# Optimization experiments

Measured on AMD Instinct MI355X. Metric: run time of the kernel, lower is better.

The kernel has to match this reference:

```python
import jax, jax.numpy as jnp
import numpy as np

B, L1, L2, H = 8, 384, 384, 128


def _lin(k, out_f, in_f, scale=0.05):
    kw, kb = jax.random.split(k)
    return (jax.random.normal(kw, (out_f, in_f), jnp.float32) * scale,
            jax.random.normal(kb, (out_f,), jnp.float32) * scale)


def setup_inputs() -> dict:
    key = jax.random.key(0)
    ks = jax.random.split(key, 10)
    Wq_w, Wq_b = _lin(ks[2], H, H)
    Wup_w, Wup_b = _lin(ks[3], H, H)
    Wvp_w, Wvp_b = _lin(ks[4], H, H)
    V_w, V_b = _lin(ks[5], 1, H)
    Wg_w, Wg_b = _lin(ks[6], 2 * H, 2 * H)
    W_ih, b_ih = _lin(ks[7], 4 * H, 2 * H)
    W_hh, b_hh = _lin(ks[8], 4 * H, H)
    return {
        "x": jax.random.normal(ks[0], (B, L1, H), jnp.float32),
        "x_mask": jnp.zeros((B, L1), dtype=bool),
        "y": jax.random.normal(ks[1], (B, L2, H), jnp.float32),
        "y_mask": jnp.zeros((B, L2), dtype=bool),
        "Wq_w": Wq_w, "Wq_b": Wq_b,
        "Wup_w": Wup_w, "Wup_b": Wup_b,
        "Wvp_w": Wvp_w, "Wvp_b": Wvp_b,
        "V_w": V_w, "V_b": V_b,
        "Wg_w": Wg_w, "Wg_b": Wg_b,
        "W_ih": W_ih, "W_hh": W_hh, "b_ih": b_ih, "b_hh": b_hh,
    }


def reference(x, x_mask, y, y_mask, Wq_w, Wq_b, Wup_w, Wup_b, Wvp_w, Wvp_b,
              V_w, V_b, Wg_w, Wg_b, W_ih, W_hh, b_ih, b_hh):
    b, l1, h = x.shape
    # projections (torch Linear: x @ W.T + b)
    x_proj = x @ Wup_w.T + Wup_b                      # [B, L1, H]
    y_proj = y @ Wq_w.T + Wq_b                        # [B, L2, H]
    # source feeds a constant zero hidden state into W_vp -> just its bias
    hidden_proj = jnp.zeros((h,), x.dtype) @ Wvp_w.T + Wvp_b  # [H]
    # additive attention scores: V . tanh(xp + yp + hp)
    sum_batch = jnp.tanh(x_proj[:, :, None, :] + y_proj[:, None, :, :] + hidden_proj)  # [B,L1,L2,H]
    s = jnp.einsum('btjh,h->btj', sum_batch, V_w[0]) + V_b[0]  # [B, L1, L2]
    # sum_mask = (1 - x_mask) outer (1 - y_mask)
    xm = 1.0 - x_mask.astype(s.dtype)
    ym = 1.0 - y_mask.astype(s.dtype)
    s = s * (xm[:, :, None] * ym[:, None, :])
    s = jnp.where(y_mask[:, None, :], -jnp.inf, s)
    alpha = jax.nn.softmax(s, axis=-1)                # [B, L1, L2]
    ct = jnp.einsum('btj,bjh->bth', alpha, y)         # [B, L1, H]
    merge = jnp.concatenate([x, ct], axis=2)          # [B, L1, 2H]
    gt = jax.nn.sigmoid(merge @ Wg_w.T + Wg_b)
    lstm_in = gt * merge                              # [B, L1, 2H]
    # single-layer unidirectional LSTM (torch gate order: i, f, g, o)
    gates_x = lstm_in @ W_ih.T + b_ih                 # [B, L1, 4H]

    def step(carry, gx):
        h_t, c_t = carry
        g = gx + h_t @ W_hh.T + b_hh
        i, f, gg, o = jnp.split(g, 4, axis=-1)
        c_n = jax.nn.sigmoid(f) * c_t + jax.nn.sigmoid(i) * jnp.tanh(gg)
        h_n = jax.nn.sigmoid(o) * jnp.tanh(c_n)
        return (h_n, c_n), h_n

    init = (jnp.zeros((b, h), x.dtype), jnp.zeros((b, h), x.dtype))
    _, hs = jax.lax.scan(step, init, jnp.swapaxes(gates_x, 0, 1))  # [L1, B, H]
    return jnp.swapaxes(hs, 0, 1)                     # [B, L1, H]
```

## Files before the change

### kernel.cpp

```cpp
#include <hip/hip_runtime.h>
#include <hip/hip_bf16.h>
#include <math.h>

typedef __attribute__((ext_vector_type(4))) float  float4v;
typedef __attribute__((ext_vector_type(2))) float  float2v;
typedef __attribute__((ext_vector_type(8))) short  short8;

#define B_ 8
#define L_ 384
#define H_ 128

__device__ __forceinline__ float bflo(unsigned int u){ unsigned int t = u << 16; float f; __builtin_memcpy(&f,&t,4); return f; }
__device__ __forceinline__ unsigned short f2bf(float f){
  unsigned int t; __builtin_memcpy(&t,&f,4);
  return (unsigned short)((t + 0x7fffu + ((t>>16)&1u)) >> 16);
}
__device__ __forceinline__ float fsig(float x){ return __fdividef(1.f, 1.f + __expf(-x)); }

__device__ __forceinline__ void barrier_lds(){
  asm volatile("s_waitcnt lgkmcnt(0)\n\ts_barrier" ::: "memory");
}

template<int K>
__device__ __forceinline__ void mfma_rowgemm_body(
    unsigned short* in_s,
    const float* __restrict__ inA, const float* __restrict__ inB,
    const float* __restrict__ W, const float* __restrict__ bias,
    const float* __restrict__ bias2, float* __restrict__ out,
    int Ntotal, int act, int row0, int ob)
{
  constexpr int KP = K + 2;
  const int tid  = threadIdx.x;
  const int w    = tid >> 6;
  const int l    = tid & 63;
  const int c    = l & 15;
  const int quad = l >> 4;

  #pragma unroll
  for (int it = 0; it < K/32; ++it) {
    int idx = it*256 + tid;
    int r = idx / (K/4);
    int k = (idx % (K/4)) * 4;
    float4v f;
    if (inB != nullptr && k >= 128)
      f = *(const float4v*)(inB + (size_t)(row0+r)*128 + (k-128));
    else if (inB != nullptr)
      f = *(const float4v*)(inA + (size_t)(row0+r)*128 + k);
    else
      f = *(const float4v*)(inA + (size_t)(row0+r)*K + k);
    unsigned int p0 = (unsigned int)f2bf(f.x) | ((unsigned int)f2bf(f.y) << 16);
    unsigned int p1 = (unsigned int)f2bf(f.z) | ((unsigned int)f2bf(f.w) << 16);
    *(unsigned int*)&in_s[r*KP + k]     = p0;
    *(unsigned int*)&in_s[r*KP + k + 2] = p1;
  }

  const int n = ob + w*16 + c;
  short8 bfr[K/32];
  #pragma unroll
  for (int kt = 0; kt < K/32; ++kt) {
    const float* src = W + (size_t)n*K + kt*32 + quad*8;
    float4v f0 = *(const float4v*)(src);
    float4v f1 = *(const float4v*)(src + 4);
    short8 v;
    v[0]=(short)f2bf(f0[0]); v[1]=(short)f2bf(f0[1]); v[2]=(short)f2bf(f0[2]); v[3]=(short)f2bf(f0[3]);
    v[4]=(short)f2bf(f1[0]); v[5]=(short)f2bf(f1[1]); v[6]=(short)f2bf(f1[2]); v[7]=(short)f2bf(f1[3]);
    bfr[kt] = v;
  }
  __syncthreads();

  const float4v z4 = {0.f,0.f,0.f,0.f};
  float4v acc0 = z4, acc1 = z4;
  #pragma unroll
  for (int kt = 0; kt < K/32; ++kt) {
    short8 a0 = *(const short8*)&in_s[(c     )*KP + kt*32 + quad*8];
    short8 a1 = *(const short8*)&in_s[(16 + c)*KP + kt*32 + quad*8];
    acc0 = __builtin_amdgcn_mfma_f32_16x16x32_bf16(a0, bfr[kt], acc0, 0,0,0);
    acc1 = __builtin_amdgcn_mfma_f32_16x16x32_bf16(a1, bfr[kt], acc1, 0,0,0);
  }

  const float C2 = 2.8853900817779268f;
  float bv = bias[n] + (bias2 ? bias2[n] : 0.f);
  #pragma unroll
  for (int mt = 0; mt < 2; ++mt) {
    float4v A = mt ? acc1 : acc0;
    #pragma unroll
    for (int r = 0; r < 4; ++r) {
      int m = mt*16 + quad*4 + r;
      float val = A[r] + bv;
      if (act == 2) {
        float mg = bflo((unsigned int)in_s[m*KP + n]);
        val = fsig(val) * mg;
      }
      if (act == 4)
        val = __builtin_amdgcn_exp2f(C2 * val);
      if (act == 3)
        out[(size_t)(row0+m)*Ntotal + (n & 127)*4 + (n >> 7)] = val;
      else
        out[(size_t)(row0+m)*Ntotal + n] = val;
    }
  }
}

template<int K>
__global__ __launch_bounds__(256) void mfma_rowgemm_kernel(
    const float* __restrict__ inA, const float* __restrict__ inB,
    const float* __restrict__ W, const float* __restrict__ bias,
    const float* __restrict__ bias2, float* __restrict__ out,
    int Ntotal, int act)
{
  __shared__ __align__(16) unsigned short in_s[32*(K+2)];
  mfma_rowgemm_body<K>(in_s, inA, inB, W, bias, bias2, out,
                       Ntotal, act, blockIdx.x*32, blockIdx.y*64);
}

__global__ __launch_bounds__(256) void proj_mfma_kernel(
    const float* __restrict__ x, const float* __restrict__ y,
    const float* __restrict__ Wup_w, const float* __restrict__ Wup_b,
    const float* __restrict__ Wq_w, const float* __restrict__ Wq_b,
    const float* __restrict__ Wvp_b,
    float* __restrict__ xp, float* __restrict__ yp)
{
  __shared__ __align__(16) unsigned short in_s[32*130];
  int bx = blockIdx.x;
  if (bx < 192)
    mfma_rowgemm_body<128>(in_s, x, nullptr, Wup_w, Wup_b, nullptr,
                           xp, 128, 4, (bx>>1)*32, (bx&1)*64);
  else {
    bx -= 192;
    mfma_rowgemm_body<128>(in_s, y, nullptr, Wq_w, Wq_b, Wvp_b,
                           yp, 128, 4, (bx>>1)*32, (bx&1)*64);
  }
}

__global__ __launch_bounds__(256) void attn_kernel(
    const float* __restrict__ xp, const float* __restrict__ yp,
    const float* __restrict__ y, const unsigned char* __restrict__ xmask,
    const unsigned char* __restrict__ ymask, const float* __restrict__ Vw,
    const float* __restrict__ Vb,
    float* __restrict__ ctp0, float* __restrict__ ctp1,
    float* __restrict__ ml)
{
  __shared__ __align__(16) float xp_s[8][128];
  __shared__ __align__(16) float v2_s[128];
  __shared__ __align__(16) float yp_s[32][132];
  __shared__ __align__(16) float yc_s[32][132];
  __shared__ float xm_s[8];
  __shared__ float ym_s[32];
  __shared__ float sv_s;
  const int tid = threadIdx.x;
  const int b   = blockIdx.y;
  const int t0  = blockIdx.x * 8;
  const int jh  = blockIdx.z;
  {
    int r = tid >> 5, k4 = (tid & 31) * 4;
    float4v f = *(const float4v*)(xp + ((size_t)(b*L_ + t0 + r))*H_ + k4);
    *(float4v*)&xp_s[r][k4] = f;
    if (tid < 32) {
      float4v v = *(const float4v*)(Vw + tid*4);
      float4v v2; v2[0]=2.f*v[0]; v2[1]=2.f*v[1]; v2[2]=2.f*v[2]; v2[3]=2.f*v[3];
      *(float4v*)&v2_s[tid*4] = v2;
    }
    if (tid < 8) xm_s[tid] = xmask[b*L_ + t0 + tid] ? 0.f : 1.f;
  }
  __syncthreads();
  if (tid < 32) {
    float4v v = *(const float4v*)&v2_s[tid*4];
    float sm = (v[0]+v[1]) + (v[2]+v[3]);
    #pragma unroll
    for (int off = 16; off >= 1; off >>= 1) sm += __shfl_xor(sm, off);
    if (tid == 0) sv_s = 0.5f*sm + Vb[0];
  }

  float4v rp[4], ry[4];
  unsigned char ymb = 0;
  {
    #pragma unroll
    for (int it = 0; it < 4; ++it) {
      int idx = it*256 + tid; int r = idx >> 5; int k4 = (idx & 31) * 4;
      size_t base = ((size_t)(b*L_ + jh*192 + r))*H_ + k4;
      rp[it] = *(const float4v*)(yp + base);
      ry[it] = *(const float4v*)(y + base);
    }
    if (tid < 32) ymb = ymask[b*L_ + jh*192 + tid];
  }

  const int t = tid >> 5, u = tid & 31;
  float mrun = -__builtin_inff(), lrun = 0.f;
  float a0=0.f, a1=0.f, a2=0.f, a3=0.f;
  float svc = 0.f, xmv = 0.f;

  for (int c = 0; c < 6; ++c) {
    __syncthreads();
    #pragma unroll
    for (int it = 0; it < 4; ++it) {
      int idx = it*256 + tid; int r = idx >> 5; int k4 = (idx & 31) * 4;
      *(float4v*)&yp_s[r][k4] = rp[it];
      *(float4v*)&yc_s[r][k4] = ry[it];
    }
    if (tid < 32) ym_s[tid] = ymb ? 0.f : 1.f;
    __syncthreads();
    if (c == 0) { svc = sv_s; xmv = xm_s[t]; }
    if (c < 5) {
      #pragma unroll
      for (int it = 0; it < 4; ++it) {
        int idx = it*256 + tid; int r = idx >> 5; int k4 = (idx & 31) * 4;
        size_t base = ((size_t)(b*L_ + jh*192 + (c+1)*32 + r))*H_ + k4;
        rp[it] = *(const float4v*)(yp + base);
        ry[it] = *(const float4v*)(y + base);
      }
      if (tid < 32) ymb = ymask[b*L_ + jh*192 + (c+1)*32 + tid];
    }

    float sA = 0.f, sB = 0.f;
    {
      const float* yr = yp_s[u];
      const float* xr = xp_s[t];
      #pragma unroll 4
      for (int k = 0; k < 128; k += 4) {
        float4v yv = *(const float4v*)&yr[k];
        float4v xv = *(const float4v*)&xr[k];
        float4v vv = *(const float4v*)&v2_s[k];
        sA -= vv[0] * __builtin_amdgcn_rcpf(__builtin_fmaf(xv[0], yv[0], 1.f));
        sB -= vv[1] * __builtin_amdgcn_rcpf(__builtin_fmaf(xv[1], yv[1], 1.f));
        sA -= vv[2] * __builtin_amdgcn_rcpf(__builtin_fmaf(xv[2], yv[2], 1.f));
        sB -= vv[3] * __builtin_amdgcn_rcpf(__builtin_fmaf(xv[3], yv[3], 1.f));
      }
    }
    float ymv = ym_s[u];
    float s = (svc + sA + sB) * xmv * ymv;
    if (ymv == 0.f) s = -__builtin_inff();
    float mc = s;
    #pragma unroll
    for (int off = 16; off >= 1; off >>= 1) mc = fmaxf(mc, __shfl_xor(mc, off));
    float mnew = fmaxf(mrun, mc);
    float p  = __expf(s - mnew);
    float sc = __expf(mrun - mnew);
    float ps = p;
    #pragma unroll
    for (int off = 16; off >= 1; off >>= 1) ps += __shfl_xor(ps, off);
    lrun = lrun * sc + ps;
    mrun = mnew;
    a0 *= sc; a1 *= sc; a2 *= sc; a3 *= sc;
    #pragma unroll 8
    for (int j = 0; j < 32; ++j) {
      float pv = __shfl(p, j, 32);
      float4v yv = *(const float4v*)&yc_s[j][u*4];
      a0 += pv*yv[0]; a1 += pv*yv[1]; a2 += pv*yv[2]; a3 += pv*yv[3];
    }
  }
  const int row = b*L_ + t0 + t;
  float* ctp = jh ? ctp1 : ctp0;
  float4v ov; ov[0]=a0; ov[1]=a1; ov[2]=a2; ov[3]=a3;
  *(float4v*)(ctp + (size_t)row*H_ + u*4) = ov;
  if (u == 0) {
    ml[(jh*2+0)*3072 + row] = mrun;
    ml[(jh*2+1)*3072 + row] = lrun;
  }
}

__global__ __launch_bounds__(256) void attn_merge_kernel(
    const float* __restrict__ ctp0, const float* __restrict__ ctp1,
    const float* __restrict__ ml, float* __restrict__ ct)
{
  const int tid = threadIdx.x;
  const int row = blockIdx.x*8 + (tid >> 5);
  const int c4  = (tid & 31) * 4;
  float m0 = ml[row],        l0 = ml[3072 + row];
  float m1 = ml[2*3072+row], l1 = ml[3*3072 + row];
  float m  = fmaxf(m0, m1);
  float e0 = __expf(m0 - m), e1 = __expf(m1 - m);
  float inv = __fdividef(1.f, l0*e0 + l1*e1);
  float4v v0 = *(const float4v*)(ctp0 + (size_t)row*H_ + c4);
  float4v v1 = *(const float4v*)(ctp1 + (size_t)row*H_ + c4);
  float4v r;
  r[0] = (v0[0]*e0 + v1[0]*e1)*inv;
  r[1] = (v0[1]*e0 + v1[1]*e1)*inv;
  r[2] = (v0[2]*e0 + v1[2]*e1)*inv;
  r[3] = (v0[3]*e0 + v1[3]*e1)*inv;
  *(float4v*)(ct + (size_t)row*H_ + c4) = r;
}

__global__ __launch_bounds__(512) void lstm_kernel(
    const float* __restrict__ gx, const float* __restrict__ Whh,
    float* __restrict__ out)
{
  __shared__ __align__(16) unsigned short h_s[2][128];
  const int tid  = threadIdx.x;
  const int b    = blockIdx.x;
  const int w    = tid >> 6;
  const int l    = tid & 63;
  const int col  = l & 15;
  const int quad = l >> 4;

  short8 bf[4][4];
  #pragma unroll
  for (int nt = 0; nt < 4; ++nt) {
    const int n = nt*128 + w*16 + col;
    #pragma unroll
    for (int kt = 0; kt < 4; ++kt) {
      const int k0 = kt*32 + quad*8;
      const float* src = Whh + (size_t)n*H_ + k0;
      float4v f0 = *(const float4v*)(src);
      float4v f1 = *(const float4v*)(src + 4);
      short8 v;
      v[0]=(short)f2bf(f0[0]); v[1]=(short)f2bf(f0[1]); v[2]=(short)f2bf(f0[2]); v[3]=(short)f2bf(f0[3]);
      v[4]=(short)f2bf(f1[0]); v[5]=(short)f2bf(f1[1]); v[6]=(short)f2bf(f1[2]); v[7]=(short)f2bf(f1[3]);
      bf[nt][kt] = v;
    }
  }

  if (tid < 128) { h_s[0][tid] = 0; h_s[1][tid] = 0; }
  float cst = 0.f;
  const int goff = w*16 + col;
  const float* gbase = gx + (size_t)b*L_*512 + goff*4;
  float* outp = out + (size_t)b*L_*H_ + goff;
  float4v gbuf[4];
  #pragma unroll
  for (int s = 0; s < 4; ++s)
    gbuf[s] = *(const float4v*)(gbase + (size_t)s*512);
  const float4v z4 = {0.f,0.f,0.f,0.f};
  const float NL2E = -1.4426950408889634f;
  const float P2L2E = 2.8853900817779268f;
  __syncthreads();

  for (int t4 = 0; t4 < L_; t4 += 4) {
    #pragma unroll
    for (int s = 0; s < 4; ++s) {
      const int tstep = t4 + s;
      const unsigned short* hb = h_s[s & 1];
      short8 a[4];
      #pragma unroll
      for (int kt=0;kt<4;++kt) a[kt] = *(const short8*)&hb[kt*32 + quad*8];
      float4v c0 = z4, c1 = z4, c2 = z4, c3 = z4;
      #pragma unroll
      for (int kt=0;kt<4;++kt) {
        c0 = __builtin_amdgcn_mfma_f32_16x16x32_bf16(a[kt], bf[0][kt], c0, 0,0,0);
        c1 = __builtin_amdgcn_mfma_f32_16x16x32_bf16(a[kt], bf[1][kt], c1, 0,0,0);
        c2 = __builtin_amdgcn_mfma_f32_16x16x32_bf16(a[kt], bf[2][kt], c2, 0,0,0);
        c3 = __builtin_amdgcn_mfma_f32_16x16x32_bf16(a[kt], bf[3][kt], c3, 0,0,0);
      }
      float g0 = c0[0] + gbuf[s][0];
      float g1 = c1[0] + gbuf[s][1];
      float g2 = c2[0] + gbuf[s][2];
      float g3 = c3[0] + gbuf[s][3];
      if (tstep + 4 < L_)
        gbuf[s] = *(const float4v*)(gbase + (size_t)(tstep+4)*512);
      if (quad == 0) {
        float ig = __builtin_amdgcn_rcpf(1.f + __builtin_amdgcn_exp2f(NL2E*g0));
        float fg = __builtin_amdgcn_rcpf(1.f + __builtin_amdgcn_exp2f(NL2E*g1));
        float gg = 1.f - 2.f*__builtin_amdgcn_rcpf(__builtin_amdgcn_exp2f(P2L2E*g2) + 1.f);
        float og = __builtin_amdgcn_rcpf(1.f + __builtin_amdgcn_exp2f(NL2E*g3));
        cst = fg*cst + ig*gg;
        float hn = og * (1.f - 2.f*__builtin_amdgcn_rcpf(__builtin_amdgcn_exp2f(P2L2E*cst) + 1.f));
        outp[(size_t)tstep*H_] = hn;
        h_s[(s+1)&1][goff] = f2bf(hn);
      }
      barrier_lds();
    }
  }
}

extern "C" void kernel_launch(void* const* d_in, const int* in_sizes, int n_in,
                              void* d_out, int out_size, void* d_ws, size_t ws_size,
                              hipStream_t stream)
{
  (void)in_sizes; (void)n_in; (void)out_size; (void)ws_size;
  const float* x     = (const float*)d_in[0];
  const unsigned char* xm = (const unsigned char*)d_in[1];
  const float* y     = (const float*)d_in[2];
  const unsigned char* ym = (const unsigned char*)d_in[3];
  const float* Wq_w  = (const float*)d_in[4];
  const float* Wq_b  = (const float*)d_in[5];
  const float* Wup_w = (const float*)d_in[6];
  const float* Wup_b = (const float*)d_in[7];
  const float* Wvp_b = (const float*)d_in[9];
  const float* V_w   = (const float*)d_in[10];
  const float* V_b   = (const float*)d_in[11];
  const float* Wg_w  = (const float*)d_in[12];
  const float* Wg_b  = (const float*)d_in[13];
  const float* W_ih  = (const float*)d_in[14];
  const float* W_hh  = (const float*)d_in[15];
  const float* b_ih  = (const float*)d_in[16];
  const float* b_hh  = (const float*)d_in[17];
  float* out = (float*)d_out;

  float* wsf    = (float*)d_ws;
  float* xp_ws  = wsf;
  float* yp_ws  = xp_ws + 393216;
  float* ct_ws  = yp_ws + 393216;
  float* li_ws  = ct_ws + 393216;
  float* gx_ws  = li_ws + 786432;
  float* ct2_ws = gx_ws + 1572864;
  float* ml_ws  = ct2_ws + 393216;

  proj_mfma_kernel<<<dim3(384),256,0,stream>>>(x, y, Wup_w, Wup_b, Wq_w, Wq_b, Wvp_b, xp_ws, yp_ws);
  attn_kernel<<<dim3(48,8,2),256,0,stream>>>(xp_ws, yp_ws, y, xm, ym, V_w, V_b, ct_ws, ct2_ws, ml_ws);
  attn_merge_kernel<<<dim3(384),256,0,stream>>>(ct_ws, ct2_ws, ml_ws, ct_ws);
  mfma_rowgemm_kernel<256><<<dim3(96,4),256,0,stream>>>(x, ct_ws, Wg_w, Wg_b, nullptr, li_ws, 256, 2);
  mfma_rowgemm_kernel<256><<<dim3(96,8),256,0,stream>>>(li_ws, nullptr, W_ih, b_ih, b_hh, gx_ws, 512, 3);
  lstm_kernel<<<dim3(8),512,0,stream>>>(gx_ws, W_hh, out);
}
```

Measured before the change: 338.1 us.

## Split attention over four key chunks and fuse partial merge into gate GEMM

The attention kernel now splits the key dimension into four chunks of 96 instead of two of 192, which doubles the grid to raise parallelism. The separate merge kernel is removed, and the gate GEMM now combines the four partial softmax results (max, sum and partial context) while loading its input tile. This removes one launch and one round trip of the context through memory, at the cost of more partial buffers and redundant merge arithmetic in the gate loads. li_ws now reuses the xp buffer to save workspace.

```diff
diff --git a/kernel.cpp b/kernel.cpp
--- a/kernel.cpp
+++ b/kernel.cpp
@@ -24,7 +24,7 @@
 template<int K>
 __device__ __forceinline__ void mfma_rowgemm_body(
     unsigned short* in_s,
-    const float* __restrict__ inA, const float* __restrict__ inB,
+    const float* __restrict__ inA,
     const float* __restrict__ W, const float* __restrict__ bias,
     const float* __restrict__ bias2, float* __restrict__ out,
     int Ntotal, int act, int row0, int ob)
@@ -41,13 +41,7 @@
     int idx = it*256 + tid;
     int r = idx / (K/4);
     int k = (idx % (K/4)) * 4;
-    float4v f;
-    if (inB != nullptr && k >= 128)
-      f = *(const float4v*)(inB + (size_t)(row0+r)*128 + (k-128));
-    else if (inB != nullptr)
-      f = *(const float4v*)(inA + (size_t)(row0+r)*128 + k);
-    else
-      f = *(const float4v*)(inA + (size_t)(row0+r)*K + k);
+    float4v f = *(const float4v*)(inA + (size_t)(row0+r)*K + k);
     unsigned int p0 = (unsigned int)f2bf(f.x) | ((unsigned int)f2bf(f.y) << 16);
     unsigned int p1 = (unsigned int)f2bf(f.z) | ((unsigned int)f2bf(f.w) << 16);
     *(unsigned int*)&in_s[r*KP + k]     = p0;
@@ -87,10 +81,6 @@
     for (int r = 0; r < 4; ++r) {
       int m = mt*16 + quad*4 + r;
       float val = A[r] + bv;
-      if (act == 2) {
-        float mg = bflo((unsigned int)in_s[m*KP + n]);
-        val = fsig(val) * mg;
-      }
       if (act == 4)
         val = __builtin_amdgcn_exp2f(C2 * val);
       if (act == 3)
@@ -103,13 +93,13 @@
 
 template<int K>
 __global__ __launch_bounds__(256) void mfma_rowgemm_kernel(
-    const float* __restrict__ inA, const float* __restrict__ inB,
+    const float* __restrict__ inA,
     const float* __restrict__ W, const float* __restrict__ bias,
     const float* __restrict__ bias2, float* __restrict__ out,
     int Ntotal, int act)
 {
   __shared__ __align__(16) unsigned short in_s[32*(K+2)];
-  mfma_rowgemm_body<K>(in_s, inA, inB, W, bias, bias2, out,
+  mfma_rowgemm_body<K>(in_s, inA, W, bias, bias2, out,
                        Ntotal, act, blockIdx.x*32, blockIdx.y*64);
 }
 
@@ -123,11 +113,11 @@
   __shared__ __align__(16) unsigned short in_s[32*130];
   int bx = blockIdx.x;
   if (bx < 192)
-    mfma_rowgemm_body<128>(in_s, x, nullptr, Wup_w, Wup_b, nullptr,
+    mfma_rowgemm_body<128>(in_s, x, Wup_w, Wup_b, nullptr,
                            xp, 128, 4, (bx>>1)*32, (bx&1)*64);
   else {
     bx -= 192;
-    mfma_rowgemm_body<128>(in_s, y, nullptr, Wq_w, Wq_b, Wvp_b,
+    mfma_rowgemm_body<128>(in_s, y, Wq_w, Wq_b, Wvp_b,
                            yp, 128, 4, (bx>>1)*32, (bx&1)*64);
   }
 }
@@ -137,8 +127,7 @@
     const float* __restrict__ y, const unsigned char* __restrict__ xmask,
     const unsigned char* __restrict__ ymask, const float* __restrict__ Vw,
     const float* __restrict__ Vb,
-    float* __restrict__ ctp0, float* __restrict__ ctp1,
-    float* __restrict__ ml)
+    float* __restrict__ ctpbase, float* __restrict__ ml)
 {
   __shared__ __align__(16) float xp_s[8][128];
   __shared__ __align__(16) float v2_s[128];
@@ -151,6 +140,7 @@
   const int b   = blockIdx.y;
   const int t0  = blockIdx.x * 8;
   const int jh  = blockIdx.z;
+  const int jb  = jh * 96;
   {
     int r = tid >> 5, k4 = (tid & 31) * 4;
     float4v f = *(const float4v*)(xp + ((size_t)(b*L_ + t0 + r))*H_ + k4);
@@ -177,11 +167,11 @@
     #pragma unroll
     for (int it = 0; it < 4; ++it) {
       int idx = it*256 + tid; int r = idx >> 5; int k4 = (idx & 31) * 4;
-      size_t base = ((size_t)(b*L_ + jh*192 + r))*H_ + k4;
+      size_t base = ((size_t)(b*L_ + jb + r))*H_ + k4;
       rp[it] = *(const float4v*)(yp + base);
       ry[it] = *(const float4v*)(y + base);
     }
-    if (tid < 32) ymb = ymask[b*L_ + jh*192 + tid];
+    if (tid < 32) ymb = ymask[b*L_ + jb + tid];
   }
 
   const int t = tid >> 5, u = tid & 31;
@@ -189,7 +179,7 @@
   float a0=0.f, a1=0.f, a2=0.f, a3=0.f;
   float svc = 0.f, xmv = 0.f;
 
-  for (int c = 0; c < 6; ++c) {
+  for (int c = 0; c < 3; ++c) {
     __syncthreads();
     #pragma unroll
     for (int it = 0; it < 4; ++it) {
@@ -200,15 +190,15 @@
     if (tid < 32) ym_s[tid] = ymb ? 0.f : 1.f;
     __syncthreads();
     if (c == 0) { svc = sv_s; xmv = xm_s[t]; }
-    if (c < 5) {
+    if (c < 2) {
       #pragma unroll
       for (int it = 0; it < 4; ++it) {
         int idx = it*256 + tid; int r = idx >> 5; int k4 = (idx & 31) * 4;
-        size_t base = ((size_t)(b*L_ + jh*192 + (c+1)*32 + r))*H_ + k4;
+        size_t base = ((size_t)(b*L_ + jb + (c+1)*32 + r))*H_ + k4;
         rp[it] = *(const float4v*)(yp + base);
         ry[it] = *(const float4v*)(y + base);
       }
-      if (tid < 32) ymb = ymask[b*L_ + jh*192 + (c+1)*32 + tid];
+      if (tid < 32) ymb = ymask[b*L_ + jb + (c+1)*32 + tid];
     }
 
     float sA = 0.f, sB = 0.f;
@@ -249,7 +239,7 @@
     }
   }
   const int row = b*L_ + t0 + t;
-  float* ctp = jh ? ctp1 : ctp0;
+  float* ctp = ctpbase + (size_t)jh*393216;
   float4v ov; ov[0]=a0; ov[1]=a1; ov[2]=a2; ov[3]=a3;
   *(float4v*)(ctp + (size_t)row*H_ + u*4) = ov;
   if (u == 0) {
@@ -258,26 +248,92 @@
   }
 }
 
-__global__ __launch_bounds__(256) void attn_merge_kernel(
-    const float* __restrict__ ctp0, const float* __restrict__ ctp1,
-    const float* __restrict__ ml, float* __restrict__ ct)
-{
-  const int tid = threadIdx.x;
-  const int row = blockIdx.x*8 + (tid >> 5);
-  const int c4  = (tid & 31) * 4;
-  float m0 = ml[row],        l0 = ml[3072 + row];
-  float m1 = ml[2*3072+row], l1 = ml[3*3072 + row];
-  float m  = fmaxf(m0, m1);
-  float e0 = __expf(m0 - m), e1 = __expf(m1 - m);
-  float inv = __fdividef(1.f, l0*e0 + l1*e1);
-  float4v v0 = *(const float4v*)(ctp0 + (size_t)row*H_ + c4);
-  float4v v1 = *(const float4v*)(ctp1 + (size_t)row*H_ + c4);
-  float4v r;
-  r[0] = (v0[0]*e0 + v1[0]*e1)*inv;
-  r[1] = (v0[1]*e0 + v1[1]*e1)*inv;
-  r[2] = (v0[2]*e0 + v1[2]*e1)*inv;
-  r[3] = (v0[3]*e0 + v1[3]*e1)*inv;
-  *(float4v*)(ct + (size_t)row*H_ + c4) = r;
+__global__ __launch_bounds__(256) void gate1_kernel(
+    const float* __restrict__ x,
+    const float* __restrict__ ctpbase, const float* __restrict__ ml,
+    const float* __restrict__ Wg_w, const float* __restrict__ Wg_b,
+    float* __restrict__ out)
+{
+  constexpr int K = 256, KP = 258;
+  __shared__ __align__(16) unsigned short in_s[32*KP];
+  const int tid  = threadIdx.x;
+  const int w    = tid >> 6;
+  const int l    = tid & 63;
+  const int c    = l & 15;
+  const int quad = l >> 4;
+  const int row0 = blockIdx.x * 32;
+  const int ob   = blockIdx.y * 64;
+
+  #pragma unroll
+  for (int it = 0; it < 8; ++it) {
+    int idx = it*256 + tid;
+    int r = idx >> 6;
+    int k = (idx & 63) * 4;
+    int row = row0 + r;
+    float4v f;
+    if (k < 128) {
+      f = *(const float4v*)(x + (size_t)row*128 + k);
+    } else {
+      float m0 = ml[       row], l0 = ml[  3072 + row];
+      float m1 = ml[2*3072+row], l1 = ml[3*3072 + row];
+      float m2 = ml[4*3072+row], l2 = ml[5*3072 + row];
+      float m3 = ml[6*3072+row], l3 = ml[7*3072 + row];
+      float mm = fmaxf(fmaxf(m0, m1), fmaxf(m2, m3));
+      float e0 = __expf(m0-mm), e1 = __expf(m1-mm);
+      float e2 = __expf(m2-mm), e3 = __expf(m3-mm);
+      float inv = __fdividef(1.f, (l0*e0 + l1*e1) + (l2*e2 + l3*e3));
+      size_t off = (size_t)row*128 + (k-128);
+      float4v v0 = *(const float4v*)(ctpbase             + off);
+      float4v v1 = *(const float4v*)(ctpbase +   393216  + off);
+      float4v v2 = *(const float4v*)(ctpbase + 2*393216  + off);
+      float4v v3 = *(const float4v*)(ctpbase + 3*393216  + off);
+      f[0] = ((v0[0]*e0 + v1[0]*e1) + (v2[0]*e2 + v3[0]*e3))*inv;
+      f[1] = ((v0[1]*e0 + v1[1]*e1) + (v2[1]*e2 + v3[1]*e3))*inv;
+      f[2] = ((v0[2]*e0 + v1[2]*e1) + (v2[2]*e2 + v3[2]*e3))*inv;
+      f[3] = ((v0[3]*e0 + v1[3]*e1) + (v2[3]*e2 + v3[3]*e3))*inv;
+    }
+    unsigned int p0 = (unsigned int)f2bf(f[0]) | ((unsigned int)f2bf(f[1]) << 16);
+    unsigned int p1 = (unsigned int)f2bf(f[2]) | ((unsigned int)f2bf(f[3]) << 16);
+    *(unsigned int*)&in_s[r*KP + k]     = p0;
+    *(unsigned int*)&in_s[r*KP + k + 2] = p1;
+  }
+
+  const int n = ob + w*16 + c;
+  short8 bfr[8];
+  #pragma unroll
+  for (int kt = 0; kt < 8; ++kt) {
+    const float* src = Wg_w + (size_t)n*K + kt*32 + quad*8;
+    float4v f0 = *(const float4v*)(src);
+    float4v f1 = *(const float4v*)(src + 4);
+    short8 v;
+    v[0]=(short)f2bf(f0[0]); v[1]=(short)f2bf(f0[1]); v[2]=(short)f2bf(f0[2]); v[3]=(short)f2bf(f0[3]);
+    v[4]=(short)f2bf(f1[0]); v[5]=(short)f2bf(f1[1]); v[6]=(short)f2bf(f1[2]); v[7]=(short)f2bf(f1[3]);
+    bfr[kt] = v;
+  }
+  __syncthreads();
+
+  const float4v z4 = {0.f,0.f,0.f,0.f};
+  float4v acc0 = z4, acc1 = z4;
+  #pragma unroll
+  for (int kt = 0; kt < 8; ++kt) {
+    short8 a0 = *(const short8*)&in_s[(c     )*KP + kt*32 + quad*8];
+    short8 a1 = *(const short8*)&in_s[(16 + c)*KP + kt*32 + quad*8];
+    acc0 = __builtin_amdgcn_mfma_f32_16x16x32_bf16(a0, bfr[kt], acc0, 0,0,0);
+    acc1 = __builtin_amdgcn_mfma_f32_16x16x32_bf16(a1, bfr[kt], acc1, 0,0,0);
+  }
+
+  float bv = Wg_b[n];
+  #pragma unroll
+  for (int mt = 0; mt < 2; ++mt) {
+    float4v A = mt ? acc1 : acc0;
+    #pragma unroll
+    for (int r = 0; r < 4; ++r) {
+      int m = mt*16 + quad*4 + r;
+      float val = A[r] + bv;
+      float mg = bflo((unsigned int)in_s[m*KP + n]);
+      out[(size_t)(row0+m)*256 + n] = fsig(val) * mg;
+    }
+  }
 }
 
 __global__ __launch_bounds__(512) void lstm_kernel(
@@ -387,16 +443,14 @@
   float* wsf    = (float*)d_ws;
   float* xp_ws  = wsf;
   float* yp_ws  = xp_ws + 393216;
-  float* ct_ws  = yp_ws + 393216;
-  float* li_ws  = ct_ws + 393216;
-  float* gx_ws  = li_ws + 786432;
-  float* ct2_ws = gx_ws + 1572864;
-  float* ml_ws  = ct2_ws + 393216;
+  float* li_ws  = xp_ws;
+  float* ctp_ws = yp_ws + 393216;
+  float* gx_ws  = ctp_ws + 4*393216;
+  float* ml_ws  = gx_ws + 1572864;
 
   proj_mfma_kernel<<<dim3(384),256,0,stream>>>(x, y, Wup_w, Wup_b, Wq_w, Wq_b, Wvp_b, xp_ws, yp_ws);
-  attn_kernel<<<dim3(48,8,2),256,0,stream>>>(xp_ws, yp_ws, y, xm, ym, V_w, V_b, ct_ws, ct2_ws, ml_ws);
-  attn_merge_kernel<<<dim3(384),256,0,stream>>>(ct_ws, ct2_ws, ml_ws, ct_ws);
-  mfma_rowgemm_kernel<256><<<dim3(96,4),256,0,stream>>>(x, ct_ws, Wg_w, Wg_b, nullptr, li_ws, 256, 2);
-  mfma_rowgemm_kernel<256><<<dim3(96,8),256,0,stream>>>(li_ws, nullptr, W_ih, b_ih, b_hh, gx_ws, 512, 3);
+  attn_kernel<<<dim3(48,8,4),256,0,stream>>>(xp_ws, yp_ws, y, xm, ym, V_w, V_b, ctp_ws, ml_ws);
+  gate1_kernel<<<dim3(96,4),256,0,stream>>>(x, ctp_ws, ml_ws, Wg_w, Wg_b, li_ws);
+  mfma_rowgemm_kernel<256><<<dim3(96,8),256,0,stream>>>(li_ws, W_ih, b_ih, b_hh, gx_ws, 512, 3);
   lstm_kernel<<<dim3(8),512,0,stream>>>(gx_ws, W_hh, out);
 }
```

Result: no change. 336.6 us (-0.5%).
